# Kernel optimization log

Hardware: AMD Instinct MI355X
Metric: run time of the kernel (lower is better)

Reference implementation:

```python
import jax, jax.numpy as jnp
from jax import lax
import numpy as np

S, B, I, H, O = 65536, 1, 2, 128, 1


def setup_inputs() -> dict:
    key = jax.random.key(0)
    k1, k2, k3, k4 = jax.random.split(key, 4)
    # xavier_normal-style scales
    s_ih = (2.0 / (4 * H + I)) ** 0.5
    s_hh = (2.0 / (4 * H + H)) ** 0.5
    s_out = (2.0 / (H + O)) ** 0.5
    return {
        "x": jax.random.normal(k1, (S, B, I), jnp.float32),
        "h0": jnp.zeros((1, B, H), jnp.float32),
        "c0": jnp.zeros((1, B, H), jnp.float32),
        "W_ih": jax.random.normal(k2, (4 * H, I), jnp.float32) * s_ih,
        "W_hh": jax.random.normal(k3, (4 * H, H), jnp.float32) * s_hh,
        "b_ih": jnp.zeros((4 * H,), jnp.float32),
        "b_hh": jnp.zeros((4 * H,), jnp.float32),
        "W_out": jax.random.normal(k4, (O, H), jnp.float32) * s_out,
        "b_out": jnp.zeros((O,), jnp.float32),
    }


def reference(x, h0, c0, W_ih, W_hh, b_ih, b_hh, W_out, b_out):
    # Precompute input-to-gate projections for all timesteps: (S, B, 4H)
    xg = jnp.einsum("sbi,gi->sbg", x, W_ih) + b_ih + b_hh

    def step(carry, xg_t):
        h, c = carry  # (B, H) each
        gates = xg_t + h @ W_hh.T  # (B, 4H); PyTorch order i,f,g,o
        i, f, g, o = jnp.split(gates, 4, axis=-1)
        i = jax.nn.sigmoid(i)
        f = jax.nn.sigmoid(f)
        g = jnp.tanh(g)
        o = jax.nn.sigmoid(o)
        c = f * c + i * g
        h = o * jnp.tanh(c)
        return (h, c), h

    (_, _), hs = lax.scan(step, (h0[0], c0[0]), xg)  # hs: (S, B, H)
    out = jnp.tanh(hs.transpose(1, 0, 2))  # (B, S, H), matches permute(1,0,2)
    out = out @ W_out.T + b_out  # (B, S, O)
    return out.reshape(out.shape[0] * out.shape[1], -1)  # (B*S, O)
```

## Files before the change

### kernel.cpp

```cpp
#include <hip/hip_runtime.h>


#define S_LEN 65536
#define HDIM 128

typedef _Float16 half2_t __attribute__((ext_vector_type(2)));
typedef _Float16 half8_t __attribute__((ext_vector_type(8)));
typedef float f32x4 __attribute__((ext_vector_type(4)));

__device__ __forceinline__ float sigm(float x) {
    return 1.0f / (1.0f + __expf(-x));
}
__device__ __forceinline__ float tanh_fast(float x) {
    return 2.0f / (1.0f + __expf(-2.0f * x)) - 1.0f;
}
__device__ __forceinline__ float dot2(half2_t a, half2_t b, float c) {
#if __has_builtin(__builtin_amdgcn_fdot2)
    return __builtin_amdgcn_fdot2(a, b, c, false);
#else
    return fmaf((float)a.x, (float)b.x, fmaf((float)a.y, (float)b.y, c));
#endif
}

__device__ __forceinline__ void block_sync_lds() {
    asm volatile("s_waitcnt lgkmcnt(0)" ::: "memory");
    __builtin_amdgcn_s_barrier();
}

__global__ __launch_bounds__(512)
__attribute__((amdgpu_waves_per_eu(2, 2)))
void lstm_seq_mfma(const float* __restrict__ x,
                   const float* __restrict__ h0,
                   const float* __restrict__ c0,
                   const float* __restrict__ W_ih,
                   const float* __restrict__ W_hh,
                   const float* __restrict__ b_ih,
                   const float* __restrict__ b_hh,
                   _Float16* __restrict__ h_hist)
{
    __shared__ __align__(16) _Float16 h_sh16[HDIM];
    __shared__ __align__(16) float gates_sh[4 * HDIM];

    const int tid  = threadIdx.x;
    const int lane = tid & 63;
    const int w    = tid >> 6;
    const int m    = lane & 15;
    const int quad = lane >> 4;

#define LOAD_AF(i, q) \
    half8_t af_##i##_##q; { \
        const float* s_ = W_hh + (size_t)(w * 64 + 16 * (i) + m) * HDIM \
                               + 32 * (q) + 8 * quad; \
        af_##i##_##q = (half8_t){ \
            (_Float16)s_[0], (_Float16)s_[1], (_Float16)s_[2], (_Float16)s_[3], \
            (_Float16)s_[4], (_Float16)s_[5], (_Float16)s_[6], (_Float16)s_[7] }; \
        asm volatile("" : "+v"(af_##i##_##q)); }
    LOAD_AF(0, 0) LOAD_AF(0, 1) LOAD_AF(0, 2) LOAD_AF(0, 3)
    LOAD_AF(1, 0) LOAD_AF(1, 1) LOAD_AF(1, 2) LOAD_AF(1, 3)
    LOAD_AF(2, 0) LOAD_AF(2, 1) LOAD_AF(2, 2) LOAD_AF(2, 3)
    LOAD_AF(3, 0) LOAD_AF(3, 1) LOAD_AF(3, 2) LOAD_AF(3, 3)
#undef LOAD_AF

    float wi0x = 0.f, wi0y = 0.f, bs0 = 0.f;
    float wi1x = 0.f, wi1y = 0.f, bs1 = 0.f;
    float wi2x = 0.f, wi2y = 0.f, bs2 = 0.f;
    float wi3x = 0.f, wi3y = 0.f, bs3 = 0.f;
    float c = 0.0f;
    if (tid < HDIM) {
        wi0x = W_ih[2 * tid];            wi0y = W_ih[2 * tid + 1];
        wi1x = W_ih[2 * (tid + 128)];    wi1y = W_ih[2 * (tid + 128) + 1];
        wi2x = W_ih[2 * (tid + 256)];    wi2y = W_ih[2 * (tid + 256) + 1];
        wi3x = W_ih[2 * (tid + 384)];    wi3y = W_ih[2 * (tid + 384) + 1];
        bs0 = b_ih[tid]       + b_hh[tid];
        bs1 = b_ih[tid + 128] + b_hh[tid + 128];
        bs2 = b_ih[tid + 256] + b_hh[tid + 256];
        bs3 = b_ih[tid + 384] + b_hh[tid + 384];
        c = c0[tid];
        h_sh16[tid] = (_Float16)h0[tid];
    }
    __syncthreads();

    const float2* xp = (const float2*)x;
    float2 xcur = {0.f, 0.f}, xnext = {0.f, 0.f};
    if (tid < HDIM) xcur = xp[0];

    half8_t bf0 = (half8_t){0,0,0,0,0,0,0,0};
    half8_t bf1 = bf0, bf2 = bf0, bf3 = bf0;

    #pragma unroll 1
    for (int t = 0; t < S_LEN; ++t) {
        if (m == 0) {
            const half8_t* hb = (const half8_t*)h_sh16;
            bf0 = hb[quad];
            bf1 = hb[4 + quad];
            bf2 = hb[8 + quad];
            bf3 = hb[12 + quad];
        }
        f32x4 acc0 = {0.f, 0.f, 0.f, 0.f};
        f32x4 acc1 = {0.f, 0.f, 0.f, 0.f};
        f32x4 acc2 = {0.f, 0.f, 0.f, 0.f};
        f32x4 acc3 = {0.f, 0.f, 0.f, 0.f};
#define MFMA_TILE(i) \
        acc##i = __builtin_amdgcn_mfma_f32_16x16x32_f16(af_##i##_0, bf0, acc##i, 0, 0, 0); \
        acc##i = __builtin_amdgcn_mfma_f32_16x16x32_f16(af_##i##_1, bf1, acc##i, 0, 0, 0); \
        acc##i = __builtin_amdgcn_mfma_f32_16x16x32_f16(af_##i##_2, bf2, acc##i, 0, 0, 0); \
        acc##i = __builtin_amdgcn_mfma_f32_16x16x32_f16(af_##i##_3, bf3, acc##i, 0, 0, 0);
        MFMA_TILE(0) MFMA_TILE(1) MFMA_TILE(2) MFMA_TILE(3)
#undef MFMA_TILE
        if (m == 0) {
            f32x4* gp = (f32x4*)gates_sh + w * 16 + quad;
            gp[0]  = acc0;
            gp[4]  = acc1;
            gp[8]  = acc2;
            gp[12] = acc3;
        }

        if (tid < HDIM) {
            const int tn = (t + 1 < S_LEN) ? (t + 1) : (S_LEN - 1);
            xnext = xp[tn];
        }
        block_sync_lds();

        if (tid < HDIM) {
            float gi = sigm(gates_sh[tid]
                            + fmaf(wi0x, xcur.x, fmaf(wi0y, xcur.y, bs0)));
            float gf = sigm(gates_sh[tid + 128]
                            + fmaf(wi1x, xcur.x, fmaf(wi1y, xcur.y, bs1)));
            float gg = tanh_fast(gates_sh[tid + 256]
                            + fmaf(wi2x, xcur.x, fmaf(wi2y, xcur.y, bs2)));
            float go = sigm(gates_sh[tid + 384]
                            + fmaf(wi3x, xcur.x, fmaf(wi3y, xcur.y, bs3)));
            c = fmaf(gf, c, gi * gg);
            float h = go * tanh_fast(c);
            _Float16 hf = (_Float16)h;
            h_sh16[tid] = hf;
            h_hist[t * HDIM + tid] = hf;
            xcur = xnext;
        }
        block_sync_lds();
    }
}

__global__ __launch_bounds__(256)
void out_proj(const _Float16* __restrict__ h_hist,
              const float* __restrict__ W_out,
              const float* __restrict__ b_out,
              float* __restrict__ out)
{
    const int lane  = threadIdx.x & 63;
    const int gwave = (blockIdx.x * 256 + threadIdx.x) >> 6;
    const int nwave = (gridDim.x * 256) >> 6;

    const float wo0 = W_out[2 * lane + 0];
    const float wo1 = W_out[2 * lane + 1];
    const float bout = b_out[0];

    for (int t = gwave; t < S_LEN; t += nwave) {
        half2_t hv = ((const half2_t*)(h_hist + t * HDIM))[lane];
        float p = tanh_fast((float)hv.x) * wo0 + tanh_fast((float)hv.y) * wo1;
        #pragma unroll
        for (int off = 32; off > 0; off >>= 1)
            p += __shfl_xor(p, off, 64);
        if (lane == 0) out[t] = p + bout;
    }
}

#define H_HI_OFF 144
__global__ __launch_bounds__(1024)
__attribute__((amdgpu_waves_per_eu(4, 4)))
void lstm_seq_full(const float* __restrict__ x,
                   const float* __restrict__ h0,
                   const float* __restrict__ c0,
                   const float* __restrict__ W_ih,
                   const float* __restrict__ W_hh,
                   const float* __restrict__ b_ih,
                   const float* __restrict__ b_hh,
                   const float* __restrict__ W_out,
                   const float* __restrict__ b_out,
                   float* __restrict__ out)
{
    __shared__ __align__(16) unsigned char h_raw[2 * H_HI_OFF];
    __shared__ float gates_part[2 * 512];
    __shared__ float red_sh[2];

    const int tid  = threadIdx.x;
    const int j    = tid >> 1;
    const int half = tid & 1;

    const float2* wr2 = (const float2*)(W_hh + j * HDIM + half * 64);
#define WDEF(i) half2_t W##i; { float2 t = wr2[i]; \
        W##i.x = (_Float16)t.x; W##i.y = (_Float16)t.y; } \
        asm volatile("" : "+v"(W##i));
    WDEF(0)  WDEF(1)  WDEF(2)  WDEF(3)  WDEF(4)  WDEF(5)  WDEF(6)  WDEF(7)
    WDEF(8)  WDEF(9)  WDEF(10) WDEF(11) WDEF(12) WDEF(13) WDEF(14) WDEF(15)
    WDEF(16) WDEF(17) WDEF(18) WDEF(19) WDEF(20) WDEF(21) WDEF(22) WDEF(23)
    WDEF(24) WDEF(25) WDEF(26) WDEF(27) WDEF(28) WDEF(29) WDEF(30) WDEF(31)
#undef WDEF

    float wih0 = 0.0f, wih1 = 0.0f, bias = 0.0f;
    if (half == 0) {
        wih0 = W_ih[2 * j + 0];
        wih1 = W_ih[2 * j + 1];
        bias = b_ih[j] + b_hh[j];
    }

    float c = 0.0f, wout = 0.0f;
    _Float16* hw = (_Float16*)(h_raw + ((tid < 64) ? 2 * tid
                                                   : H_HI_OFF + 2 * (tid - 64)));
    if (tid < HDIM) {
        c = c0[tid];
        wout = W_out[tid];
        *hw = (_Float16)h0[tid];
    }
    const float bout = b_out[0];
    __syncthreads();

    const float2* xp = (const float2*)x;
    float2 xcur = xp[0];
    const half8_t* hp = (const half8_t*)(h_raw + half * H_HI_OFF);

    #pragma unroll 1
    for (int t = 0; t < S_LEN; ++t) {
        const int tn = (t + 1 < S_LEN) ? (t + 1) : (S_LEN - 1);
        float2 xnext = xp[tn];

        float a0 = fmaf(wih0, xcur.x, fmaf(wih1, xcur.y, bias));
        float a1 = 0.0f, a2 = 0.0f, a3 = 0.0f;

#define CHUNK(cc, w0_, w1_, w2_, w3_) {                         \
        half8_t hv = hp[cc];                                    \
        half2_t p0 = { hv[0], hv[1] };                          \
        half2_t p1 = { hv[2], hv[3] };                          \
        half2_t p2 = { hv[4], hv[5] };                          \
        half2_t p3 = { hv[6], hv[7] };                          \
        a0 = dot2(w0_, p0, a0);                                 \
        a1 = dot2(w1_, p1, a1);                                 \
        a2 = dot2(w2_, p2, a2);                                 \
        a3 = dot2(w3_, p3, a3); }
        CHUNK(0, W0,  W1,  W2,  W3)
        CHUNK(1, W4,  W5,  W6,  W7)
        CHUNK(2, W8,  W9,  W10, W11)
        CHUNK(3, W12, W13, W14, W15)
        CHUNK(4, W16, W17, W18, W19)
        CHUNK(5, W20, W21, W22, W23)
        CHUNK(6, W24, W25, W26, W27)
        CHUNK(7, W28, W29, W30, W31)
#undef CHUNK

        gates_part[half * 512 + j] = (a0 + a1) + (a2 + a3);
        __syncthreads();

        if (tid < HDIM) {
            float gi = sigm(gates_part[tid]            + gates_part[tid + 512]);
            float gf = sigm(gates_part[tid + 128]      + gates_part[tid + 640]);
            float gg = tanh_fast(gates_part[tid + 256] + gates_part[tid + 768]);
            float go = sigm(gates_part[tid + 384]      + gates_part[tid + 896]);
            c = fmaf(gf, c, gi * gg);
            float h = go * tanh_fast(c);
            *hw = (_Float16)h;

            float p = tanh_fast(h) * wout;
            #pragma unroll
            for (int off = 32; off > 0; off >>= 1)
                p += __shfl_xor(p, off, 64);
            if ((tid & 63) == 0) red_sh[tid >> 6] = p;
        }
        __syncthreads();

        if (tid == 0) out[t] = red_sh[0] + red_sh[1] + bout;
        xcur = xnext;
    }
}

extern "C" void kernel_launch(void* const* d_in, const int* in_sizes, int n_in,
                              void* d_out, int out_size, void* d_ws, size_t ws_size,
                              hipStream_t stream) {
    const float* x     = (const float*)d_in[0];
    const float* h0    = (const float*)d_in[1];
    const float* c0    = (const float*)d_in[2];
    const float* W_ih  = (const float*)d_in[3];
    const float* W_hh  = (const float*)d_in[4];
    const float* b_ih  = (const float*)d_in[5];
    const float* b_hh  = (const float*)d_in[6];
    const float* W_out = (const float*)d_in[7];
    const float* b_out = (const float*)d_in[8];

    const size_t need = (size_t)S_LEN * HDIM * sizeof(_Float16);
    if (ws_size >= need) {
        _Float16* h_hist = (_Float16*)d_ws;
        lstm_seq_mfma<<<dim3(1), dim3(512), 0, stream>>>(
            x, h0, c0, W_ih, W_hh, b_ih, b_hh, h_hist);
        out_proj<<<dim3(1024), dim3(256), 0, stream>>>(
            h_hist, W_out, b_out, (float*)d_out);
    } else {
        lstm_seq_full<<<dim3(1), dim3(1024), 0, stream>>>(
            x, h0, c0, W_ih, W_hh, b_ih, b_hh, W_out, b_out, (float*)d_out);
    }
}
```

Measured before the change: 47.01 ms.

## Compute LSTM cell updates in MFMA lanes, double-buffer h, one barrier per step

Remaps the W_hh rows so each wave holds the i, f, g and o rows for the same 16 hidden units. Each MFMA output lane can then apply the gate nonlinearities and the cell update directly, with no gates round trip through shared memory. The input projection and bias are folded into the accumulator initialisation, and h is double-buffered in LDS, cutting the per-timestep barriers from two to one. The cost is redundant activation math in lanes whose results are discarded, plus extra per-lane register state.

```diff
diff --git a/kernel.cpp b/kernel.cpp
--- a/kernel.cpp
+++ b/kernel.cpp
@@ -1,10 +1,10 @@
 #include <hip/hip_runtime.h>
-
 
 #define S_LEN 65536
 #define HDIM 128
 
 typedef _Float16 half2_t __attribute__((ext_vector_type(2)));
+typedef _Float16 half4_t __attribute__((ext_vector_type(4)));
 typedef _Float16 half8_t __attribute__((ext_vector_type(8)));
 typedef float f32x4 __attribute__((ext_vector_type(4)));
 
@@ -38,8 +38,7 @@
                    const float* __restrict__ b_hh,
                    _Float16* __restrict__ h_hist)
 {
-    __shared__ __align__(16) _Float16 h_sh16[HDIM];
-    __shared__ __align__(16) float gates_sh[4 * HDIM];
+    __shared__ __align__(16) _Float16 hbuf[2][HDIM];
 
     const int tid  = threadIdx.x;
     const int lane = tid & 63;
@@ -47,96 +46,98 @@
     const int m    = lane & 15;
     const int quad = lane >> 4;
 
-#define LOAD_AF(i, q) \
-    half8_t af_##i##_##q; { \
-        const float* s_ = W_hh + (size_t)(w * 64 + 16 * (i) + m) * HDIM \
-                               + 32 * (q) + 8 * quad; \
-        af_##i##_##q = (half8_t){ \
+#define LOAD_AF(g, kc) \
+    half8_t af_##g##_##kc; { \
+        const float* s_ = W_hh + (size_t)((g) * 128 + 16 * w + m) * HDIM \
+                               + 32 * (kc) + 8 * quad; \
+        af_##g##_##kc = (half8_t){ \
             (_Float16)s_[0], (_Float16)s_[1], (_Float16)s_[2], (_Float16)s_[3], \
             (_Float16)s_[4], (_Float16)s_[5], (_Float16)s_[6], (_Float16)s_[7] }; \
-        asm volatile("" : "+v"(af_##i##_##q)); }
+        asm volatile("" : "+v"(af_##g##_##kc)); }
     LOAD_AF(0, 0) LOAD_AF(0, 1) LOAD_AF(0, 2) LOAD_AF(0, 3)
     LOAD_AF(1, 0) LOAD_AF(1, 1) LOAD_AF(1, 2) LOAD_AF(1, 3)
     LOAD_AF(2, 0) LOAD_AF(2, 1) LOAD_AF(2, 2) LOAD_AF(2, 3)
     LOAD_AF(3, 0) LOAD_AF(3, 1) LOAD_AF(3, 2) LOAD_AF(3, 3)
 #undef LOAD_AF
 
-    float wi0x = 0.f, wi0y = 0.f, bs0 = 0.f;
-    float wi1x = 0.f, wi1y = 0.f, bs1 = 0.f;
-    float wi2x = 0.f, wi2y = 0.f, bs2 = 0.f;
-    float wi3x = 0.f, wi3y = 0.f, bs3 = 0.f;
-    float c = 0.0f;
-    if (tid < HDIM) {
-        wi0x = W_ih[2 * tid];            wi0y = W_ih[2 * tid + 1];
-        wi1x = W_ih[2 * (tid + 128)];    wi1y = W_ih[2 * (tid + 128) + 1];
-        wi2x = W_ih[2 * (tid + 256)];    wi2y = W_ih[2 * (tid + 256) + 1];
-        wi3x = W_ih[2 * (tid + 384)];    wi3y = W_ih[2 * (tid + 384) + 1];
-        bs0 = b_ih[tid]       + b_hh[tid];
-        bs1 = b_ih[tid + 128] + b_hh[tid + 128];
-        bs2 = b_ih[tid + 256] + b_hh[tid + 256];
-        bs3 = b_ih[tid + 384] + b_hh[tid + 384];
-        c = c0[tid];
-        h_sh16[tid] = (_Float16)h0[tid];
-    }
+    const int base = 16 * w + 4 * quad;
+#define PBC(g) \
+    f32x4 wx##g = {0,0,0,0}, wy##g = {0,0,0,0}, bs##g = {0,0,0,0}; \
+    if (m == 0) { \
+        _Pragma("unroll") \
+        for (int r = 0; r < 4; ++r) { \
+            int row = (g) * 128 + base + r; \
+            wx##g[r] = W_ih[2 * row]; \
+            wy##g[r] = W_ih[2 * row + 1]; \
+            bs##g[r] = b_ih[row] + b_hh[row]; \
+        } \
+        asm volatile("" : "+v"(wx##g), "+v"(wy##g), "+v"(bs##g)); \
+    }
+    PBC(0) PBC(1) PBC(2) PBC(3)
+#undef PBC
+
+    f32x4 c = {0, 0, 0, 0};
+    if (m == 0) {
+        #pragma unroll
+        for (int r = 0; r < 4; ++r) c[r] = c0[base + r];
+    }
+
+    if (tid < HDIM) hbuf[0][tid] = (_Float16)h0[tid];
     __syncthreads();
 
     const float2* xp = (const float2*)x;
-    float2 xcur = {0.f, 0.f}, xnext = {0.f, 0.f};
-    if (tid < HDIM) xcur = xp[0];
+    float2 xcur = xp[0];
 
     half8_t bf0 = (half8_t){0,0,0,0,0,0,0,0};
     half8_t bf1 = bf0, bf2 = bf0, bf3 = bf0;
 
     #pragma unroll 1
     for (int t = 0; t < S_LEN; ++t) {
+        const int p = t & 1;
+        const int tn = (t + 1 < S_LEN) ? (t + 1) : (S_LEN - 1);
+        float2 xnext = xp[tn];
+
         if (m == 0) {
-            const half8_t* hb = (const half8_t*)h_sh16;
+            const half8_t* hb = (const half8_t*)hbuf[p];
             bf0 = hb[quad];
             bf1 = hb[4 + quad];
             bf2 = hb[8 + quad];
             bf3 = hb[12 + quad];
         }
-        f32x4 acc0 = {0.f, 0.f, 0.f, 0.f};
-        f32x4 acc1 = {0.f, 0.f, 0.f, 0.f};
-        f32x4 acc2 = {0.f, 0.f, 0.f, 0.f};
-        f32x4 acc3 = {0.f, 0.f, 0.f, 0.f};
-#define MFMA_TILE(i) \
-        acc##i = __builtin_amdgcn_mfma_f32_16x16x32_f16(af_##i##_0, bf0, acc##i, 0, 0, 0); \
-        acc##i = __builtin_amdgcn_mfma_f32_16x16x32_f16(af_##i##_1, bf1, acc##i, 0, 0, 0); \
-        acc##i = __builtin_amdgcn_mfma_f32_16x16x32_f16(af_##i##_2, bf2, acc##i, 0, 0, 0); \
-        acc##i = __builtin_amdgcn_mfma_f32_16x16x32_f16(af_##i##_3, bf3, acc##i, 0, 0, 0);
+
+        f32x4 acc0, acc1, acc2, acc3;
+        #pragma unroll
+        for (int r = 0; r < 4; ++r) {
+            acc0[r] = fmaf(wx0[r], xcur.x, fmaf(wy0[r], xcur.y, bs0[r]));
+            acc1[r] = fmaf(wx1[r], xcur.x, fmaf(wy1[r], xcur.y, bs1[r]));
+            acc2[r] = fmaf(wx2[r], xcur.x, fmaf(wy2[r], xcur.y, bs2[r]));
+            acc3[r] = fmaf(wx3[r], xcur.x, fmaf(wy3[r], xcur.y, bs3[r]));
+        }
+
+#define MFMA_TILE(g) \
+        acc##g = __builtin_amdgcn_mfma_f32_16x16x32_f16(af_##g##_0, bf0, acc##g, 0, 0, 0); \
+        acc##g = __builtin_amdgcn_mfma_f32_16x16x32_f16(af_##g##_1, bf1, acc##g, 0, 0, 0); \
+        acc##g = __builtin_amdgcn_mfma_f32_16x16x32_f16(af_##g##_2, bf2, acc##g, 0, 0, 0); \
+        acc##g = __builtin_amdgcn_mfma_f32_16x16x32_f16(af_##g##_3, bf3, acc##g, 0, 0, 0);
         MFMA_TILE(0) MFMA_TILE(1) MFMA_TILE(2) MFMA_TILE(3)
 #undef MFMA_TILE
+
+        half4_t hv4;
+        #pragma unroll
+        for (int r = 0; r < 4; ++r) {
+            float gi = sigm(acc0[r]);
+            float gf = sigm(acc1[r]);
+            float gg = tanh_fast(acc2[r]);
+            float go = sigm(acc3[r]);
+            c[r] = fmaf(gf, c[r], gi * gg);
+            hv4[r] = (_Float16)(go * tanh_fast(c[r]));
+        }
         if (m == 0) {
-            f32x4* gp = (f32x4*)gates_sh + w * 16 + quad;
-            gp[0]  = acc0;
-            gp[4]  = acc1;
-            gp[8]  = acc2;
-            gp[12] = acc3;
-        }
-
-        if (tid < HDIM) {
-            const int tn = (t + 1 < S_LEN) ? (t + 1) : (S_LEN - 1);
-            xnext = xp[tn];
-        }
-        block_sync_lds();
-
-        if (tid < HDIM) {
-            float gi = sigm(gates_sh[tid]
-                            + fmaf(wi0x, xcur.x, fmaf(wi0y, xcur.y, bs0)));
-            float gf = sigm(gates_sh[tid + 128]
-                            + fmaf(wi1x, xcur.x, fmaf(wi1y, xcur.y, bs1)));
-            float gg = tanh_fast(gates_sh[tid + 256]
-                            + fmaf(wi2x, xcur.x, fmaf(wi2y, xcur.y, bs2)));
-            float go = sigm(gates_sh[tid + 384]
-                            + fmaf(wi3x, xcur.x, fmaf(wi3y, xcur.y, bs3)));
-            c = fmaf(gf, c, gi * gg);
-            float h = go * tanh_fast(c);
-            _Float16 hf = (_Float16)h;
-            h_sh16[tid] = hf;
-            h_hist[t * HDIM + tid] = hf;
-            xcur = xnext;
-        }
+            *(half4_t*)&hbuf[1 - p][base] = hv4;
+            *(half4_t*)(h_hist + (size_t)t * HDIM + base) = hv4;
+        }
+
+        xcur = xnext;
         block_sync_lds();
     }
 }
@@ -156,7 +157,7 @@
     const float bout = b_out[0];
 
     for (int t = gwave; t < S_LEN; t += nwave) {
-        half2_t hv = ((const half2_t*)(h_hist + t * HDIM))[lane];
+        half2_t hv = ((const half2_t*)(h_hist + (size_t)t * HDIM))[lane];
         float p = tanh_fast((float)hv.x) * wo0 + tanh_fast((float)hv.y) * wo1;
         #pragma unroll
         for (int off = 32; off > 0; off >>= 1)
```

Measured after the change: 125.8 ms. 168% more time.

## Spread LSTM gate activations across all threads using lane shuffles

Applied to the files above, without the earlier changes.

Gate pre-activations are now stored in an interleaved layout, so each of the 512 threads computes one gate activation instead of 128 threads computing four each. Tanh is folded into the sigmoid path through a per-thread scale, and the four gates of a hidden unit are combined with xor shuffles. The hidden-state buffer is double-buffered, and every thread now loads the next input. The aim is to shorten the serial activation phase of each timestep, at the cost of extra shuffles and more redundant x loads.

```diff
diff --git a/kernel.cpp b/kernel.cpp
--- a/kernel.cpp
+++ b/kernel.cpp
@@ -1,5 +1,4 @@
 #include <hip/hip_runtime.h>
-
 
 #define S_LEN 65536
 #define HDIM 128
@@ -38,7 +37,7 @@
                    const float* __restrict__ b_hh,
                    _Float16* __restrict__ h_hist)
 {
-    __shared__ __align__(16) _Float16 h_sh16[HDIM];
+    __shared__ __align__(16) _Float16 hbuf[2][HDIM];
     __shared__ __align__(16) float gates_sh[4 * HDIM];
 
     const int tid  = threadIdx.x;
@@ -61,36 +60,32 @@
     LOAD_AF(3, 0) LOAD_AF(3, 1) LOAD_AF(3, 2) LOAD_AF(3, 3)
 #undef LOAD_AF
 
-    float wi0x = 0.f, wi0y = 0.f, bs0 = 0.f;
-    float wi1x = 0.f, wi1y = 0.f, bs1 = 0.f;
-    float wi2x = 0.f, wi2y = 0.f, bs2 = 0.f;
-    float wi3x = 0.f, wi3y = 0.f, bs3 = 0.f;
-    float c = 0.0f;
-    if (tid < HDIM) {
-        wi0x = W_ih[2 * tid];            wi0y = W_ih[2 * tid + 1];
-        wi1x = W_ih[2 * (tid + 128)];    wi1y = W_ih[2 * (tid + 128) + 1];
-        wi2x = W_ih[2 * (tid + 256)];    wi2y = W_ih[2 * (tid + 256) + 1];
-        wi3x = W_ih[2 * (tid + 384)];    wi3y = W_ih[2 * (tid + 384) + 1];
-        bs0 = b_ih[tid]       + b_hh[tid];
-        bs1 = b_ih[tid + 128] + b_hh[tid + 128];
-        bs2 = b_ih[tid + 256] + b_hh[tid + 256];
-        bs3 = b_ih[tid + 384] + b_hh[tid + 384];
-        c = c0[tid];
-        h_sh16[tid] = (_Float16)h0[tid];
-    }
+    const int cg   = tid & 3;
+    const int cr   = tid >> 2;
+    const int crow = cg * HDIM + cr;
+    const float wihx = W_ih[2 * crow];
+    const float wihy = W_ih[2 * crow + 1];
+    const float bias = b_ih[crow] + b_hh[crow];
+    const float gsc  = (cg == 2) ? 2.0f : 1.0f;
+    float c = (cg == 0) ? c0[cr] : 0.0f;
+
+    if (tid < HDIM) hbuf[0][tid] = (_Float16)h0[tid];
     __syncthreads();
 
     const float2* xp = (const float2*)x;
-    float2 xcur = {0.f, 0.f}, xnext = {0.f, 0.f};
-    if (tid < HDIM) xcur = xp[0];
+    float2 xcur = xp[0];
 
     half8_t bf0 = (half8_t){0,0,0,0,0,0,0,0};
     half8_t bf1 = bf0, bf2 = bf0, bf3 = bf0;
 
     #pragma unroll 1
     for (int t = 0; t < S_LEN; ++t) {
+        const int p  = t & 1;
+        const int tn = (t + 1 < S_LEN) ? (t + 1) : (S_LEN - 1);
+        float2 xnext = xp[tn];
+
         if (m == 0) {
-            const half8_t* hb = (const half8_t*)h_sh16;
+            const half8_t* hb = (const half8_t*)hbuf[p];
             bf0 = hb[quad];
             bf1 = hb[4 + quad];
             bf2 = hb[8 + quad];
@@ -107,36 +102,38 @@
         acc##i = __builtin_amdgcn_mfma_f32_16x16x32_f16(af_##i##_3, bf3, acc##i, 0, 0, 0);
         MFMA_TILE(0) MFMA_TILE(1) MFMA_TILE(2) MFMA_TILE(3)
 #undef MFMA_TILE
+
         if (m == 0) {
-            f32x4* gp = (f32x4*)gates_sh + w * 16 + quad;
-            gp[0]  = acc0;
-            gp[4]  = acc1;
-            gp[8]  = acc2;
-            gp[12] = acc3;
-        }
-
-        if (tid < HDIM) {
-            const int tn = (t + 1 < S_LEN) ? (t + 1) : (S_LEN - 1);
-            xnext = xp[tn];
+#define STORE_TILE(i, accv) { \
+            const int G = w * 64 + 16 * (i) + 4 * quad;        \
+            float* gp = gates_sh + ((G & 127) << 2) + (G >> 7); \
+            gp[0]  = accv[0]; \
+            gp[4]  = accv[1]; \
+            gp[8]  = accv[2]; \
+            gp[12] = accv[3]; }
+            STORE_TILE(0, acc0)
+            STORE_TILE(1, acc1)
+            STORE_TILE(2, acc2)
+            STORE_TILE(3, acc3)
+#undef STORE_TILE
         }
         block_sync_lds();
 
-        if (tid < HDIM) {
-            float gi = sigm(gates_sh[tid]
-                            + fmaf(wi0x, xcur.x, fmaf(wi0y, xcur.y, bs0)));
-            float gf = sigm(gates_sh[tid + 128]
-                            + fmaf(wi1x, xcur.x, fmaf(wi1y, xcur.y, bs1)));
-            float gg = tanh_fast(gates_sh[tid + 256]
-                            + fmaf(wi2x, xcur.x, fmaf(wi2y, xcur.y, bs2)));
-            float go = sigm(gates_sh[tid + 384]
-                            + fmaf(wi3x, xcur.x, fmaf(wi3y, xcur.y, bs3)));
-            c = fmaf(gf, c, gi * gg);
-            float h = go * tanh_fast(c);
+        float gx = gates_sh[tid]
+                 + fmaf(wihx, xcur.x, fmaf(wihy, xcur.y, bias));
+        float v   = 1.0f / (1.0f + __expf(-gsc * gx));
+        float act = fmaf(gsc, v, 1.0f - gsc);
+        float actB = __shfl_xor(act, 1, 64);
+        float actC = __shfl_xor(act, 2, 64);
+        float actD = __shfl_xor(actB, 2, 64);
+        if (cg == 0) {
+            c = fmaf(actB, c, act * actC);
+            float h = actD * tanh_fast(c);
             _Float16 hf = (_Float16)h;
-            h_sh16[tid] = hf;
-            h_hist[t * HDIM + tid] = hf;
-            xcur = xnext;
-        }
+            hbuf[1 - p][cr] = hf;
+            h_hist[(size_t)t * HDIM + cr] = hf;
+        }
+        xcur = xnext;
         block_sync_lds();
     }
 }
@@ -156,7 +153,7 @@
     const float bout = b_out[0];
 
     for (int t = gwave; t < S_LEN; t += nwave) {
-        half2_t hv = ((const half2_t*)(h_hist + t * HDIM))[lane];
+        half2_t hv = ((const half2_t*)(h_hist + (size_t)t * HDIM))[lane];
         float p = tanh_fast((float)hv.x) * wo0 + tanh_fast((float)hv.y) * wo1;
         #pragma unroll
         for (int off = 32; off > 0; off >>= 1)
```

Result: faster. 44.56 ms (-5.2%).
